# Optimization experiments

Measured on AMD Instinct MI355X. Metric: run time of the kernel, lower is better.

The kernel has to match this reference:

```python
import jax, jax.numpy as jnp
import numpy as np

L, D, H, KV, HD, KVL, I, PL = 8, 2048, 8, 2, 256, 4096, 8192, 256
FULL = (4,)          # layers with full (global) attention / global RoPE
POS = 2047           # current decode position (cache write slot)
N_REP = H // KV      # GQA expansion factor


def rms(x, eps=1e-6):
    # RMSNorm without scale (v_norm); scale applied by caller where needed
    return x * jax.lax.rsqrt(jnp.mean(x * x, axis=-1, keepdims=True) + eps)


def rope(x, cos, sin):
    half = HD // 2
    rot = jnp.concatenate([-x[..., half:], x[..., :half]], axis=-1)
    return x * cos + rot * sin


def _rope_tables(theta):
    inv = 1.0 / (theta ** (np.arange(0, HD, 2, dtype=np.float32) / HD))
    ang = jnp.asarray(POS * inv, dtype=jnp.float32)
    return jnp.concatenate([jnp.cos(ang)] * 2), jnp.concatenate([jnp.sin(ang)] * 2)


def setup_inputs() -> dict:
    key = jax.random.key(0)
    ks = jax.random.split(key, 24)
    r = lambda k, s, sc=0.02: jax.random.normal(k, s, jnp.float32) * sc
    gains = lambda k, s: 1.0 + jax.random.normal(k, s, jnp.float32) * 0.02
    cos_s, sin_s = _rope_tables(10000.0)
    cos_f, sin_f = _rope_tables(1000000.0)
    um = jnp.zeros((1, 1, KVL, 1), jnp.float32).at[0, 0, POS, 0].set(1.0)
    mask = jnp.where(jnp.arange(KVL) <= POS, 0.0, -1e9).astype(jnp.float32)
    return {
        "hidden_states": r(ks[0], (1, 1, D), 1.0),
        "causal_mask": mask,
        "update_mask": um,
        "per_layer_combined": r(ks[1], (1, 1, L * PL), 1.0),
        "cos_s": cos_s, "sin_s": sin_s, "cos_f": cos_f, "sin_f": sin_f,
        "K_in": r(ks[2], (L, KV, KVL, HD)),
        "V_in": r(ks[3], (L, KV, KVL, HD)),
        "w_q": r(ks[4], (L, H * HD, D)),
        "w_k": r(ks[5], (L, KV * HD, D)),
        "w_v": r(ks[6], (L, KV * HD, D)),
        "w_o": r(ks[7], (L, D, H * HD)),
        "g_in_ln": gains(ks[8], (L, D)),
        "g_q_norm": gains(ks[9], (L, HD)),
        "g_k_norm": gains(ks[10], (L, HD)),
        "g_post_attn_ln": gains(ks[11], (L, D)),
        "g_pre_ff_ln": gains(ks[12], (L, D)),
        "g_post_ff_ln": gains(ks[13], (L, D)),
        "w_gate": r(ks[14], (L, I, D)),
        "w_up": r(ks[15], (L, I, D)),
        "w_down": r(ks[16], (L, D, I)),
        "w_plg": r(ks[17], (L, PL, D)),
        "w_plp": r(ks[18], (L, D, PL)),
        "g_post_pl_ln": gains(ks[19], (L, D)),
        "layer_scalar": jnp.ones((L,), jnp.float32),
    }


def reference(hidden_states, causal_mask, update_mask, per_layer_combined,
              cos_s, sin_s, cos_f, sin_f, K_in, V_in,
              w_q, w_k, w_v, w_o,
              g_in_ln, g_q_norm, g_k_norm, g_post_attn_ln, g_pre_ff_ln, g_post_ff_ln,
              w_gate, w_up, w_down, w_plg, w_plp, g_post_pl_ln, layer_scalar):
    um = update_mask[0, 0]          # [KVL,1] one-hot at write position
    h = hidden_states[0, 0]         # [D], batch=1/seq=1 decode
    K_outs, V_outs = [], []
    for i in range(L):
        cos, sin = (cos_f, sin_f) if i in FULL else (cos_s, sin_s)
        # --- attention block ---
        res = h
        x = rms(h) * g_in_ln[i]
        q = rms((w_q[i] @ x).reshape(H, HD)) * g_q_norm[i]
        q = rope(q, cos, sin)                                   # [H,HD]
        k = rms((w_k[i] @ x).reshape(KV, HD)) * g_k_norm[i]
        k = rope(k, cos, sin)                                   # [KV,HD]
        v = rms((w_v[i] @ x).reshape(KV, HD))                    # v_norm (no scale)
        # full-tensor masked blend = KV cache write (faithful to source)
        Ko = K_in[i] * (1.0 - um) + k[:, None, :] * um          # [KV,KVL,HD]
        Vo = V_in[i] * (1.0 - um) + v[:, None, :] * um
        K_outs.append(Ko); V_outs.append(Vo)
        Ke = jnp.repeat(Ko, N_REP, axis=0)                      # GQA expand [H,KVL,HD]
        Ve = jnp.repeat(Vo, N_REP, axis=0)
        scores = jnp.einsum('hd,hkd->hk', q, Ke) + causal_mask  # no 1/sqrt(hd) in source
        attn = jax.nn.softmax(scores, axis=-1)
        ao = jnp.einsum('hk,hkd->hd', attn, Ve).reshape(H * HD)
        ao = rms(w_o[i] @ ao) * g_post_attn_ln[i]
        h = res + ao
        # --- gated MLP ---
        res = h
        xm = rms(h) * g_pre_ff_ln[i]
        m = w_down[i] @ (jax.nn.gelu(w_gate[i] @ xm, approximate=True) * (w_up[i] @ xm))
        h = res + rms(m) * g_post_ff_ln[i]
        # --- per-layer input gating ---
        res = h
        pls = per_layer_combined[0, 0, i * PL:(i + 1) * PL]     # [PL]
        g = jax.nn.gelu(w_plg[i] @ h, approximate=True) * pls
        h = res + rms(w_plp[i] @ g) * g_post_pl_ln[i]
        h = h * layer_scalar[i]
    return (h[None, None, :], jnp.stack(K_outs), jnp.stack(V_outs))
```

## Files before the change

kernel.cpp:

```cpp
#include <hip/hip_runtime.h>

#define NL   8
#define DIM  2048
#define NH   8
#define NKV  2
#define HD   256
#define KVL  4096
#define FFI  8192
#define PLD  256
#define POS  2047
#define NCH  16
#define CP   128

__device__ __forceinline__ float dot4(float4 a, float4 b){
  return a.x*b.x + a.y*b.y + a.z*b.z + a.w*b.w;
}

__device__ __forceinline__ float waveAllSum(float v){
#pragma unroll
  for(int o=1;o<64;o<<=1) v += __shfl_xor(v,o,64);
  return v;
}

__device__ __forceinline__ float waveAllMax(float v){
#pragma unroll
  for(int o=1;o<64;o<<=1) v = fmaxf(v, __shfl_xor(v,o,64));
  return v;
}

__device__ __forceinline__ float blockSum256(float v, float* red){
  int lane = threadIdx.x & 63, w = threadIdx.x >> 6;
  v = waveAllSum(v);
  __syncthreads();
  if(lane==0) red[w] = v;
  __syncthreads();
  return red[0]+red[1]+red[2]+red[3];
}

__device__ __forceinline__ float gelu_tanh(float v){
  return 0.5f*v*(1.0f + tanhf(0.7978845608028654f*(v + 0.044715f*v*v*v)));
}

__global__ __launch_bounds__(256) void qkv_k(
    const float* __restrict__ Wq, const float* __restrict__ Wk,
    const float* __restrict__ Wv,
    const float* __restrict__ hC, const float* __restrict__ u,
    const float* __restrict__ g_pl, const float* __restrict__ lsc,
    const float* __restrict__ g_in, const float* __restrict__ hidden,
    float* __restrict__ hA, float* __restrict__ qkv){
  __shared__ float xs[DIM];
  __shared__ float red[4];
  int tid = threadIdx.x;
  float hv[8];
  if(hidden){
#pragma unroll
    for(int i=0;i<8;i++) hv[i] = hidden[tid + i*256];
  } else {
    float uv[8]; float ss1 = 0.f;
#pragma unroll
    for(int i=0;i<8;i++){ uv[i] = u[tid + i*256]; ss1 += uv[i]*uv[i]; }
    ss1 = blockSum256(ss1, red);
    float r1 = rsqrtf(ss1*(1.f/DIM) + 1e-6f);
    float ls = lsc[0];
#pragma unroll
    for(int i=0;i<8;i++){
      int idx = tid + i*256;
      hv[i] = (hC[idx] + uv[i]*r1*g_pl[idx])*ls;
    }
  }
  float ss2 = 0.f;
#pragma unroll
  for(int i=0;i<8;i++) ss2 += hv[i]*hv[i];
  ss2 = blockSum256(ss2, red);
  float r2 = rsqrtf(ss2*(1.f/DIM) + 1e-6f);
#pragma unroll
  for(int i=0;i<8;i++){
    int idx = tid + i*256;
    xs[idx] = hv[i]*r2*g_in[idx];
    if(blockIdx.x==0) hA[idx] = hv[i];
  }
  __syncthreads();
  int lane = tid & 63, wv = tid >> 6;
  int r = blockIdx.x*4 + wv;
  const float* W; int row;
  if(r < 2048){ W = Wq; row = r; }
  else if(r < 2560){ W = Wk; row = r - 2048; }
  else { W = Wv; row = r - 2560; }
  const float4* Wr = (const float4*)(W + (size_t)row*DIM);
  const float4* xs4 = (const float4*)xs;
  float acc = 0.f;
#pragma unroll
  for(int i=0;i<DIM/256;i++) acc += dot4(Wr[lane + i*64], xs4[lane + i*64]);
  acc = waveAllSum(acc);
  if(lane==0) qkv[r] = acc;
}

__device__ __forceinline__ float4 normRope(const float* __restrict__ raw, int lane,
    const float* __restrict__ gain, const float* __restrict__ cosT,
    const float* __restrict__ sinT, bool doRope){
  float4 v4 = ((const float4*)raw)[lane];
  float ss = waveAllSum(dot4(v4,v4));
  float sc = rsqrtf(ss*(1.f/HD) + 1e-6f);
  float4 n;
  if(gain){
    float4 g4 = ((const float4*)gain)[lane];
    n.x=v4.x*sc*g4.x; n.y=v4.y*sc*g4.y; n.z=v4.z*sc*g4.z; n.w=v4.w*sc*g4.w;
  } else {
    n.x=v4.x*sc; n.y=v4.y*sc; n.z=v4.z*sc; n.w=v4.w*sc;
  }
  if(!doRope) return n;
  float4 np;
  np.x=__shfl_xor(n.x,32,64); np.y=__shfl_xor(n.y,32,64);
  np.z=__shfl_xor(n.z,32,64); np.w=__shfl_xor(n.w,32,64);
  float4 c4 = ((const float4*)cosT)[lane];
  float4 s4 = ((const float4*)sinT)[lane];
  float sg = (lane < 32) ? -1.f : 1.f;
  float4 o;
  o.x = n.x*c4.x + sg*np.x*s4.x;
  o.y = n.y*c4.y + sg*np.y*s4.y;
  o.z = n.z*c4.z + sg*np.z*s4.z;
  o.w = n.w*c4.w + sg*np.w*s4.w;
  return o;
}

__global__ __launch_bounds__(256) void attn_k(
    const float* __restrict__ qkv,
    const float* __restrict__ gq, const float* __restrict__ gk,
    const float* __restrict__ cosT, const float* __restrict__ sinT,
    float* __restrict__ Kc, float* __restrict__ Vc,
    float* __restrict__ pm, float* __restrict__ pl, float* __restrict__ po){
  int b = blockIdx.x;
  int tid = threadIdx.x, lane = tid & 63, wv = tid >> 6;

  if(b == NKV*NCH){
    int kvv = wv >> 1, isV = wv & 1;
    const float* raw = qkv + (isV ? 2560 : 2048) + kvv*HD;
    float4 o = normRope(raw, lane, isV ? nullptr : gk, cosT, sinT, !isV);
    float* dst = (isV ? Vc : Kc) + ((size_t)kvv*KVL + POS)*HD;
    ((float4*)dst)[lane] = o;
    return;
  }

  int kv = b >> 4, c = b & (NCH-1);
  __shared__ float q_s[4][HD];
  __shared__ float kf[HD], vf[HD];
  __shared__ float s_s[4][CP];
  __shared__ float s_w[4][CP];

  {
    float4 o = normRope(qkv + (kv*4 + wv)*HD, lane, gq, cosT, sinT, true);
    ((float4*)q_s[wv])[lane] = o;
  }
  bool fresh = (c == NCH-1);
  if(fresh){
    if(wv == 0){
      float4 o = normRope(qkv + 2048 + kv*HD, lane, gk, cosT, sinT, true);
      ((float4*)kf)[lane] = o;
    } else if(wv == 1){
      float4 o = normRope(qkv + 2560 + kv*HD, lane, nullptr, cosT, sinT, false);
      ((float4*)vf)[lane] = o;
    }
  }
  __syncthreads();

  float4 q4[4];
#pragma unroll
  for(int hh=0;hh<4;hh++) q4[hh] = ((const float4*)q_s[hh])[lane];
  const float4* Kp = (const float4*)(Kc + ((size_t)kv*KVL + c*CP)*HD);
  for(int j=0;j<CP/4;j++){
    int p = wv*(CP/4) + j;
    float4 k4 = (fresh && p==CP-1) ? ((const float4*)kf)[lane]
                                   : Kp[(size_t)p*64 + lane];
    float d0 = dot4(k4,q4[0]), d1 = dot4(k4,q4[1]);
    float d2 = dot4(k4,q4[2]), d3 = dot4(k4,q4[3]);
    d0 = waveAllSum(d0); d1 = waveAllSum(d1);
    d2 = waveAllSum(d2); d3 = waveAllSum(d3);
    if(lane==0){ s_s[0][p]=d0; s_s[1][p]=d1; s_s[2][p]=d2; s_s[3][p]=d3; }
  }
  __syncthreads();

  {
    float s0 = s_s[wv][lane], s1 = s_s[wv][lane+64];
    float m = waveAllMax(fmaxf(s0,s1));
    float e0 = __expf(s0-m), e1 = __expf(s1-m);
    s_w[wv][lane] = e0; s_w[wv][lane+64] = e1;
    float lsum = waveAllSum(e0+e1);
    if(lane==0){
      int hg = kv*4 + wv;
      pm[hg*NCH + c] = m;
      pl[hg*NCH + c] = lsum;
    }
  }
  __syncthreads();

  float acc[4] = {0.f,0.f,0.f,0.f};
  const float* Vp = Vc + ((size_t)kv*KVL + c*CP)*HD;
  for(int p=0;p<CP;p++){
    float vv = (fresh && p==CP-1) ? vf[tid] : Vp[(size_t)p*HD + tid];
#pragma unroll
    for(int hh=0;hh<4;hh++) acc[hh] += s_w[hh][p]*vv;
  }
#pragma unroll
  for(int hh=0;hh<4;hh++){
    int hg = kv*4 + hh;
    po[((size_t)hg*NCH + c)*HD + tid] = acc[hh];
  }
}

__global__ __launch_bounds__(256) void wo_k(const float* __restrict__ W,
    const float* __restrict__ pm, const float* __restrict__ pl,
    const float* __restrict__ po, float* __restrict__ y){
  __shared__ float ao_s[DIM];
  __shared__ float se_s[NH][NCH];
  __shared__ float Ms[NH];
  __shared__ float Li[NH];
  int tid = threadIdx.x;
  if(tid < NH){
    float m = -1e30f;
    for(int c=0;c<NCH;c++) m = fmaxf(m, pm[tid*NCH+c]);
    Ms[tid] = m;
  }
  __syncthreads();
  if(tid < NH*NCH){
    int h = tid >> 4, c = tid & (NCH-1);
    se_s[h][c] = __expf(pm[h*NCH+c] - Ms[h]);
  }
  __syncthreads();
  if(tid < NH){
    float L = 0.f;
    for(int c=0;c<NCH;c++) L += pl[tid*NCH+c]*se_s[tid][c];
    Li[tid] = 1.f/L;
  }
  __syncthreads();
  for(int h=0;h<NH;h++){
    float a = 0.f;
#pragma unroll
    for(int c=0;c<NCH;c++) a += po[((size_t)h*NCH+c)*HD + tid]*se_s[h][c];
    ao_s[h*HD + tid] = a*Li[h];
  }
  __syncthreads();
  int lane = tid & 63, wv = tid >> 6;
  int r = blockIdx.x*4 + wv;
  const float4* Wr = (const float4*)(W + (size_t)r*DIM);
  const float4* xs4 = (const float4*)ao_s;
  float acc = 0.f;
#pragma unroll
  for(int i=0;i<DIM/256;i++) acc += dot4(Wr[lane + i*64], xs4[lane + i*64]);
  acc = waveAllSum(acc);
  if(lane==0) y[r] = acc;
}

__global__ __launch_bounds__(256) void gateup_k(const float* __restrict__ Wg,
    const float* __restrict__ Wu, const float* __restrict__ y,
    const float* __restrict__ hA, const float* __restrict__ g_pa,
    const float* __restrict__ g_pf, float* __restrict__ hB, float* __restrict__ t){
  __shared__ float xs[DIM];
  __shared__ float red[4];
  int tid = threadIdx.x;
  float yv[8]; float ss1 = 0.f;
#pragma unroll
  for(int i=0;i<8;i++){ yv[i] = y[tid + i*256]; ss1 += yv[i]*yv[i]; }
  ss1 = blockSum256(ss1, red);
  float r1 = rsqrtf(ss1*(1.f/DIM) + 1e-6f);
  float hv[8]; float ss2 = 0.f;
#pragma unroll
  for(int i=0;i<8;i++){
    int idx = tid + i*256;
    hv[i] = hA[idx] + yv[i]*r1*g_pa[idx];
    ss2 += hv[i]*hv[i];
  }
  ss2 = blockSum256(ss2, red);
  float r2 = rsqrtf(ss2*(1.f/DIM) + 1e-6f);
#pragma unroll
  for(int i=0;i<8;i++){
    int idx = tid + i*256;
    xs[idx] = hv[i]*r2*g_pf[idx];
    if(blockIdx.x==0) hB[idx] = hv[i];
  }
  __syncthreads();
  int lane = tid & 63, wv = tid >> 6;
  int j = blockIdx.x*4 + wv;
  const float4* Gr = (const float4*)(Wg + (size_t)j*DIM);
  const float4* Ur = (const float4*)(Wu + (size_t)j*DIM);
  const float4* xs4 = (const float4*)xs;
  float ag = 0.f, au = 0.f;
#pragma unroll
  for(int i=0;i<DIM/256;i++){
    float4 bv = xs4[lane + i*64];
    ag += dot4(Gr[lane + i*64], bv);
    au += dot4(Ur[lane + i*64], bv);
  }
  ag = waveAllSum(ag);
  au = waveAllSum(au);
  if(lane==0) t[j] = gelu_tanh(ag)*au;
}

template<int C>
__global__ __launch_bounds__(256) void gemv_k(const float* __restrict__ W,
    const float* __restrict__ x, float* __restrict__ y){
  __shared__ float xs[C];
  for(int i=threadIdx.x; i<C/4; i+=256)
    ((float4*)xs)[i] = ((const float4*)x)[i];
  __syncthreads();
  int lane = threadIdx.x & 63, wv = threadIdx.x >> 6;
  int r = blockIdx.x*4 + wv;
  const float4* Wr = (const float4*)(W + (size_t)r*C);
  const float4* xs4 = (const float4*)xs;
  float acc = 0.f;
#pragma unroll
  for(int i=0;i<C/256;i++) acc += dot4(Wr[lane + i*64], xs4[lane + i*64]);
  acc = waveAllSum(acc);
  if(lane==0) y[r] = acc;
}

__global__ __launch_bounds__(256) void plg_k(const float* __restrict__ W,
    const float* __restrict__ mv, const float* __restrict__ hB,
    const float* __restrict__ g_ff, const float* __restrict__ pls,
    float* __restrict__ hCout, float* __restrict__ gb){
  __shared__ float xs[DIM];
  __shared__ float red[4];
  int tid = threadIdx.x;
  float mvv[8]; float ss1 = 0.f;
#pragma unroll
  for(int i=0;i<8;i++){ mvv[i] = mv[tid + i*256]; ss1 += mvv[i]*mvv[i]; }
  ss1 = blockSum256(ss1, red);
  float r1 = rsqrtf(ss1*(1.f/DIM) + 1e-6f);
#pragma unroll
  for(int i=0;i<8;i++){
    int idx = tid + i*256;
    float hc = hB[idx] + mvv[i]*r1*g_ff[idx];
    xs[idx] = hc;
    if(blockIdx.x==0) hCout[idx] = hc;
  }
  __syncthreads();
  int lane = tid & 63, wv = tid >> 6;
  int r = blockIdx.x*4 + wv;
  const float4* Wr = (const float4*)(W + (size_t)r*DIM);
  const float4* xs4 = (const float4*)xs;
  float acc = 0.f;
#pragma unroll
  for(int i=0;i<DIM/256;i++) acc += dot4(Wr[lane + i*64], xs4[lane + i*64]);
  acc = waveAllSum(acc);
  if(lane==0) gb[r] = gelu_tanh(acc)*pls[r];
}

__global__ __launch_bounds__(256) void final_k(const float* __restrict__ u,
    const float* __restrict__ hC, const float* __restrict__ g_pl,
    const float* __restrict__ lsc, float* __restrict__ out){
  __shared__ float red[4];
  int tid = threadIdx.x;
  float uv[8]; float ss1 = 0.f;
#pragma unroll
  for(int i=0;i<8;i++){ uv[i] = u[tid + i*256]; ss1 += uv[i]*uv[i]; }
  ss1 = blockSum256(ss1, red);
  float r1 = rsqrtf(ss1*(1.f/DIM) + 1e-6f);
  float ls = lsc[0];
#pragma unroll
  for(int i=0;i<8;i++){
    int idx = tid + i*256;
    out[idx] = (hC[idx] + uv[i]*r1*g_pl[idx])*ls;
  }
}

extern "C" void kernel_launch(void* const* d_in, const int* in_sizes, int n_in,
                              void* d_out, int out_size, void* d_ws, size_t ws_size,
                              hipStream_t stream){
  const float* hidden   = (const float*)d_in[0];
  const float* plc      = (const float*)d_in[3];
  const float* cos_s    = (const float*)d_in[4];
  const float* sin_s    = (const float*)d_in[5];
  const float* cos_f    = (const float*)d_in[6];
  const float* sin_f    = (const float*)d_in[7];
  const float* K_in     = (const float*)d_in[8];
  const float* V_in     = (const float*)d_in[9];
  const float* w_q      = (const float*)d_in[10];
  const float* w_k      = (const float*)d_in[11];
  const float* w_v      = (const float*)d_in[12];
  const float* w_o      = (const float*)d_in[13];
  const float* g_in_ln  = (const float*)d_in[14];
  const float* g_q_norm = (const float*)d_in[15];
  const float* g_k_norm = (const float*)d_in[16];
  const float* g_pa_ln  = (const float*)d_in[17];
  const float* g_pf_ln  = (const float*)d_in[18];
  const float* g_ff_ln  = (const float*)d_in[19];
  const float* w_gate   = (const float*)d_in[20];
  const float* w_up     = (const float*)d_in[21];
  const float* w_down   = (const float*)d_in[22];
  const float* w_plg    = (const float*)d_in[23];
  const float* w_plp    = (const float*)d_in[24];
  const float* g_pl_ln  = (const float*)d_in[25];
  const float* l_scal   = (const float*)d_in[26];

  float* out  = (float*)d_out;
  float* outK = out + DIM;
  float* outV = outK + (size_t)NL*NKV*KVL*HD;

  float* ws   = (float*)d_ws;
  float* hA   = ws;
  float* hB   = ws + 2048;
  float* hC   = ws + 4096;
  float* qkv  = ws + 6144;
  float* y    = ws + 9216;
  float* t    = ws + 11264;
  float* mv   = ws + 19456;
  float* gb   = ws + 21504;
  float* u    = ws + 21760;
  float* pm   = ws + 23808;
  float* pl   = ws + 23936;
  float* po   = ws + 24064;

  (void)hipMemcpyAsync(outK, K_in, (size_t)NL*NKV*KVL*HD*sizeof(float),
                       hipMemcpyDeviceToDevice, stream);
  (void)hipMemcpyAsync(outV, V_in, (size_t)NL*NKV*KVL*HD*sizeof(float),
                       hipMemcpyDeviceToDevice, stream);

  for(int l=0;l<NL;l++){
    const float* cosT = (l==4) ? cos_f : cos_s;
    const float* sinT = (l==4) ? sin_f : sin_s;
    float* Kl = outK + (size_t)l*NKV*KVL*HD;
    float* Vl = outV + (size_t)l*NKV*KVL*HD;

    qkv_k<<<768,256,0,stream>>>(
        w_q + (size_t)l*NH*HD*DIM, w_k + (size_t)l*NKV*HD*DIM,
        w_v + (size_t)l*NKV*HD*DIM,
        hC, u,
        (l>0) ? g_pl_ln + (size_t)(l-1)*DIM : g_pl_ln,
        (l>0) ? l_scal + (l-1) : l_scal,
        g_in_ln + (size_t)l*DIM,
        (l==0) ? hidden : nullptr,
        hA, qkv);

    attn_k<<<NKV*NCH+1,256,0,stream>>>(qkv, g_q_norm + l*HD, g_k_norm + l*HD,
                                       cosT, sinT, Kl, Vl, pm, pl, po);

    wo_k<<<512,256,0,stream>>>(w_o + (size_t)l*DIM*NH*HD, pm, pl, po, y);

    gateup_k<<<FFI/4,256,0,stream>>>(w_gate + (size_t)l*FFI*DIM,
                                     w_up + (size_t)l*FFI*DIM,
                                     y, hA, g_pa_ln + (size_t)l*DIM,
                                     g_pf_ln + (size_t)l*DIM, hB, t);

    gemv_k<FFI><<<512,256,0,stream>>>(w_down + (size_t)l*DIM*FFI, t, mv);

    plg_k<<<PLD/4,256,0,stream>>>(w_plg + (size_t)l*PLD*DIM, mv, hB,
                                  g_ff_ln + (size_t)l*DIM, plc + l*PLD, hC, gb);

    gemv_k<PLD><<<512,256,0,stream>>>(w_plp + (size_t)l*DIM*PLD, gb, u);
  }

  final_k<<<1,256,0,stream>>>(u, hC, g_pl_ln + (size_t)(NL-1)*DIM,
                              l_scal + (NL-1), out);
}
```

Measured before the change: 976.5 us.

## Split attention into finer KV chunks, separate combine kernel, prefetch weights in GEMVs

Attention now uses 128 chunks of 16 positions instead of 16 chunks of 128, which gives 257 blocks instead of 33 and spreads KV streaming across more CUs. The cross-chunk softmax combine moves out of wo_k into a new attn_c kernel, and the output projection reuses the generic GEMV. The down projection gets a dedicated kernel with one block per row split across four waves. All GEMVs now load their weight float4s into registers up front to raise memory-level parallelism. The changes add one kernel launch per layer, a larger partial-output buffer and more register pressure.

```diff
diff --git a/kernel.cpp b/kernel.cpp
--- a/kernel.cpp
+++ b/kernel.cpp
@@ -9,8 +9,8 @@
 #define FFI  8192
 #define PLD  256
 #define POS  2047
-#define NCH  16
-#define CP   128
+#define NCH  128
+#define CP   16
 
 __device__ __forceinline__ float dot4(float4 a, float4 b){
   return a.x*b.x + a.y*b.y + a.z*b.z + a.w*b.w;
@@ -19,12 +19,6 @@
 __device__ __forceinline__ float waveAllSum(float v){
 #pragma unroll
   for(int o=1;o<64;o<<=1) v += __shfl_xor(v,o,64);
-  return v;
-}
-
-__device__ __forceinline__ float waveAllMax(float v){
-#pragma unroll
-  for(int o=1;o<64;o<<=1) v = fmaxf(v, __shfl_xor(v,o,64));
   return v;
 }
 
@@ -39,60 +33,6 @@
 
 __device__ __forceinline__ float gelu_tanh(float v){
   return 0.5f*v*(1.0f + tanhf(0.7978845608028654f*(v + 0.044715f*v*v*v)));
-}
-
-__global__ __launch_bounds__(256) void qkv_k(
-    const float* __restrict__ Wq, const float* __restrict__ Wk,
-    const float* __restrict__ Wv,
-    const float* __restrict__ hC, const float* __restrict__ u,
-    const float* __restrict__ g_pl, const float* __restrict__ lsc,
-    const float* __restrict__ g_in, const float* __restrict__ hidden,
-    float* __restrict__ hA, float* __restrict__ qkv){
-  __shared__ float xs[DIM];
-  __shared__ float red[4];
-  int tid = threadIdx.x;
-  float hv[8];
-  if(hidden){
-#pragma unroll
-    for(int i=0;i<8;i++) hv[i] = hidden[tid + i*256];
-  } else {
-    float uv[8]; float ss1 = 0.f;
-#pragma unroll
-    for(int i=0;i<8;i++){ uv[i] = u[tid + i*256]; ss1 += uv[i]*uv[i]; }
-    ss1 = blockSum256(ss1, red);
-    float r1 = rsqrtf(ss1*(1.f/DIM) + 1e-6f);
-    float ls = lsc[0];
-#pragma unroll
-    for(int i=0;i<8;i++){
-      int idx = tid + i*256;
-      hv[i] = (hC[idx] + uv[i]*r1*g_pl[idx])*ls;
-    }
-  }
-  float ss2 = 0.f;
-#pragma unroll
-  for(int i=0;i<8;i++) ss2 += hv[i]*hv[i];
-  ss2 = blockSum256(ss2, red);
-  float r2 = rsqrtf(ss2*(1.f/DIM) + 1e-6f);
-#pragma unroll
-  for(int i=0;i<8;i++){
-    int idx = tid + i*256;
-    xs[idx] = hv[i]*r2*g_in[idx];
-    if(blockIdx.x==0) hA[idx] = hv[i];
-  }
-  __syncthreads();
-  int lane = tid & 63, wv = tid >> 6;
-  int r = blockIdx.x*4 + wv;
-  const float* W; int row;
-  if(r < 2048){ W = Wq; row = r; }
-  else if(r < 2560){ W = Wk; row = r - 2048; }
-  else { W = Wv; row = r - 2560; }
-  const float4* Wr = (const float4*)(W + (size_t)row*DIM);
-  const float4* xs4 = (const float4*)xs;
-  float acc = 0.f;
-#pragma unroll
-  for(int i=0;i<DIM/256;i++) acc += dot4(Wr[lane + i*64], xs4[lane + i*64]);
-  acc = waveAllSum(acc);
-  if(lane==0) qkv[r] = acc;
 }
 
 __device__ __forceinline__ float4 normRope(const float* __restrict__ raw, int lane,
@@ -123,42 +63,97 @@
   return o;
 }
 
+__global__ __launch_bounds__(256) void qkv_k(
+    const float* __restrict__ Wq, const float* __restrict__ Wk,
+    const float* __restrict__ Wv,
+    const float* __restrict__ hC, const float* __restrict__ u,
+    const float* __restrict__ g_pl, const float* __restrict__ lsc,
+    const float* __restrict__ g_in, const float* __restrict__ hidden,
+    float* __restrict__ hA, float* __restrict__ qkv){
+  __shared__ float xs[DIM];
+  __shared__ float red[4];
+  int tid = threadIdx.x;
+  float hv[8];
+  if(hidden){
+#pragma unroll
+    for(int i=0;i<8;i++) hv[i] = hidden[tid + i*256];
+  } else {
+    float uv[8]; float ss1 = 0.f;
+#pragma unroll
+    for(int i=0;i<8;i++){ uv[i] = u[tid + i*256]; ss1 += uv[i]*uv[i]; }
+    ss1 = blockSum256(ss1, red);
+    float r1 = rsqrtf(ss1*(1.f/DIM) + 1e-6f);
+    float ls = lsc[0];
+#pragma unroll
+    for(int i=0;i<8;i++){
+      int idx = tid + i*256;
+      hv[i] = (hC[idx] + uv[i]*r1*g_pl[idx])*ls;
+    }
+  }
+  float ss2 = 0.f;
+#pragma unroll
+  for(int i=0;i<8;i++) ss2 += hv[i]*hv[i];
+  ss2 = blockSum256(ss2, red);
+  float r2 = rsqrtf(ss2*(1.f/DIM) + 1e-6f);
+#pragma unroll
+  for(int i=0;i<8;i++){
+    int idx = tid + i*256;
+    xs[idx] = hv[i]*r2*g_in[idx];
+    if(blockIdx.x==0) hA[idx] = hv[i];
+  }
+  __syncthreads();
+  int lane = tid & 63, wv = tid >> 6;
+  int r = blockIdx.x*4 + wv;
+  const float* W; int row;
+  if(r < 2048){ W = Wq; row = r; }
+  else if(r < 2560){ W = Wk; row = r - 2048; }
+  else { W = Wv; row = r - 2560; }
+  const float4* Wr = (const float4*)(W + (size_t)row*DIM);
+  const float4* xs4 = (const float4*)xs;
+  float4 w8[8];
+#pragma unroll
+  for(int i=0;i<8;i++) w8[i] = Wr[i*64+lane];
+  float acc = 0.f;
+#pragma unroll
+  for(int i=0;i<8;i++) acc += dot4(w8[i], xs4[i*64+lane]);
+  acc = waveAllSum(acc);
+  if(lane==0) qkv[r] = acc;
+}
+
 __global__ __launch_bounds__(256) void attn_k(
-    const float* __restrict__ qkv,
+    const float* __restrict__ qkvb,
     const float* __restrict__ gq, const float* __restrict__ gk,
     const float* __restrict__ cosT, const float* __restrict__ sinT,
-    float* __restrict__ Kc, float* __restrict__ Vc,
+    float* __restrict__ Kl, float* __restrict__ Vl,
     float* __restrict__ pm, float* __restrict__ pl, float* __restrict__ po){
-  int b = blockIdx.x;
-  int tid = threadIdx.x, lane = tid & 63, wv = tid >> 6;
+  int b = blockIdx.x, tid = threadIdx.x, lane = tid & 63, wv = tid >> 6;
 
   if(b == NKV*NCH){
     int kvv = wv >> 1, isV = wv & 1;
-    const float* raw = qkv + (isV ? 2560 : 2048) + kvv*HD;
+    const float* raw = qkvb + (isV ? 2560 : 2048) + kvv*HD;
     float4 o = normRope(raw, lane, isV ? nullptr : gk, cosT, sinT, !isV);
-    float* dst = (isV ? Vc : Kc) + ((size_t)kvv*KVL + POS)*HD;
+    float* dst = (isV ? Vl : Kl) + ((size_t)kvv*KVL + POS)*HD;
     ((float4*)dst)[lane] = o;
     return;
   }
 
-  int kv = b >> 4, c = b & (NCH-1);
+  int kv = b & 1, c = b >> 1;
   __shared__ float q_s[4][HD];
-  __shared__ float kf[HD], vf[HD];
+  __shared__ float vf_s[HD];
   __shared__ float s_s[4][CP];
   __shared__ float s_w[4][CP];
+  bool fresh = (c == NCH-1);
 
   {
-    float4 o = normRope(qkv + (kv*4 + wv)*HD, lane, gq, cosT, sinT, true);
+    float4 o = normRope(qkvb + (kv*4 + wv)*HD, lane, gq, cosT, sinT, true);
     ((float4*)q_s[wv])[lane] = o;
   }
-  bool fresh = (c == NCH-1);
+  float4 kf4 = {0,0,0,0};
   if(fresh){
-    if(wv == 0){
-      float4 o = normRope(qkv + 2048 + kv*HD, lane, gk, cosT, sinT, true);
-      ((float4*)kf)[lane] = o;
-    } else if(wv == 1){
-      float4 o = normRope(qkv + 2560 + kv*HD, lane, nullptr, cosT, sinT, false);
-      ((float4*)vf)[lane] = o;
+    if(wv == 3) kf4 = normRope(qkvb + 2048 + kv*HD, lane, gk, cosT, sinT, true);
+    if(wv == 1){
+      float4 o = normRope(qkvb + 2560 + kv*HD, lane, nullptr, cosT, sinT, false);
+      ((float4*)vf_s)[lane] = o;
     }
   }
   __syncthreads();
@@ -166,11 +161,11 @@
   float4 q4[4];
 #pragma unroll
   for(int hh=0;hh<4;hh++) q4[hh] = ((const float4*)q_s[hh])[lane];
-  const float4* Kp = (const float4*)(Kc + ((size_t)kv*KVL + c*CP)*HD);
-  for(int j=0;j<CP/4;j++){
-    int p = wv*(CP/4) + j;
-    float4 k4 = (fresh && p==CP-1) ? ((const float4*)kf)[lane]
-                                   : Kp[(size_t)p*64 + lane];
+  const float4* Kp = (const float4*)(Kl + ((size_t)kv*KVL + c*CP)*HD);
+#pragma unroll
+  for(int j=0;j<4;j++){
+    int p = wv*4 + j;
+    float4 k4 = (fresh && p==CP-1) ? kf4 : Kp[(size_t)p*64 + lane];
     float d0 = dot4(k4,q4[0]), d1 = dot4(k4,q4[1]);
     float d2 = dot4(k4,q4[2]), d3 = dot4(k4,q4[3]);
     d0 = waveAllSum(d0); d1 = waveAllSum(d1);
@@ -179,73 +174,85 @@
   }
   __syncthreads();
 
-  {
-    float s0 = s_s[wv][lane], s1 = s_s[wv][lane+64];
-    float m = waveAllMax(fmaxf(s0,s1));
-    float e0 = __expf(s0-m), e1 = __expf(s1-m);
-    s_w[wv][lane] = e0; s_w[wv][lane+64] = e1;
-    float lsum = waveAllSum(e0+e1);
-    if(lane==0){
-      int hg = kv*4 + wv;
-      pm[hg*NCH + c] = m;
-      pl[hg*NCH + c] = lsum;
-    }
-  }
-  __syncthreads();
-
+  if(tid < 64){
+    int hh = tid >> 4, pp = tid & 15;
+    float s = s_s[hh][pp];
+    float m = s;
+#pragma unroll
+    for(int o=1;o<16;o<<=1) m = fmaxf(m, __shfl_xor(m,o,64));
+    float e = __expf(s - m);
+    float ls = e;
+#pragma unroll
+    for(int o=1;o<16;o<<=1) ls += __shfl_xor(ls,o,64);
+    s_w[hh][pp] = e;
+    if(pp==0){ int hg = kv*4 + hh; pm[hg*NCH + c] = m; pl[hg*NCH + c] = ls; }
+  }
+  __syncthreads();
+
+  int d = tid;
+  const float* Vp = Vl + ((size_t)kv*KVL + c*CP)*HD;
+  float vv[CP];
+#pragma unroll
+  for(int p2=0;p2<CP;p2++) vv[p2] = Vp[(size_t)p2*HD + d];
+  if(fresh) vv[CP-1] = vf_s[d];
   float acc[4] = {0.f,0.f,0.f,0.f};
-  const float* Vp = Vc + ((size_t)kv*KVL + c*CP)*HD;
-  for(int p=0;p<CP;p++){
-    float vv = (fresh && p==CP-1) ? vf[tid] : Vp[(size_t)p*HD + tid];
-#pragma unroll
-    for(int hh=0;hh<4;hh++) acc[hh] += s_w[hh][p]*vv;
-  }
-#pragma unroll
-  for(int hh=0;hh<4;hh++){
-    int hg = kv*4 + hh;
-    po[((size_t)hg*NCH + c)*HD + tid] = acc[hh];
-  }
-}
-
-__global__ __launch_bounds__(256) void wo_k(const float* __restrict__ W,
-    const float* __restrict__ pm, const float* __restrict__ pl,
-    const float* __restrict__ po, float* __restrict__ y){
-  __shared__ float ao_s[DIM];
-  __shared__ float se_s[NH][NCH];
-  __shared__ float Ms[NH];
-  __shared__ float Li[NH];
-  int tid = threadIdx.x;
-  if(tid < NH){
-    float m = -1e30f;
-    for(int c=0;c<NCH;c++) m = fmaxf(m, pm[tid*NCH+c]);
-    Ms[tid] = m;
-  }
-  __syncthreads();
-  if(tid < NH*NCH){
-    int h = tid >> 4, c = tid & (NCH-1);
-    se_s[h][c] = __expf(pm[h*NCH+c] - Ms[h]);
-  }
-  __syncthreads();
-  if(tid < NH){
-    float L = 0.f;
-    for(int c=0;c<NCH;c++) L += pl[tid*NCH+c]*se_s[tid][c];
-    Li[tid] = 1.f/L;
-  }
-  __syncthreads();
-  for(int h=0;h<NH;h++){
-    float a = 0.f;
-#pragma unroll
-    for(int c=0;c<NCH;c++) a += po[((size_t)h*NCH+c)*HD + tid]*se_s[h][c];
-    ao_s[h*HD + tid] = a*Li[h];
-  }
-  __syncthreads();
-  int lane = tid & 63, wv = tid >> 6;
+#pragma unroll
+  for(int p2=0;p2<CP;p2++){
+#pragma unroll
+    for(int hh=0;hh<4;hh++) acc[hh] += s_w[hh][p2]*vv[p2];
+  }
+#pragma unroll
+  for(int hh=0;hh<4;hh++)
+    po[((size_t)(kv*4+hh)*NCH + c)*HD + d] = acc[hh];
+}
+
+__global__ __launch_bounds__(256) void attn_c(const float* __restrict__ pm,
+    const float* __restrict__ pl, const float* __restrict__ po, float* __restrict__ ao){
+  int h = blockIdx.x, tid = threadIdx.x;
+  __shared__ float sm[NCH], sl[NCH], se[NCH];
+  if(tid < NCH){ sm[tid] = pm[h*NCH+tid]; sl[tid] = pl[h*NCH+tid]; }
+  __syncthreads();
+  float M = -1e30f;
+  for(int c=0;c<NCH;c++) M = fmaxf(M, sm[c]);
+  if(tid < NCH) se[tid] = __expf(sm[tid]-M);
+  __syncthreads();
+  float Lh = 0.f;
+  for(int c=0;c<NCH;c++) Lh += sl[c]*se[c];
+  float a0=0.f, a1=0.f, a2=0.f, a3=0.f;
+#pragma unroll 1
+  for(int c=0;c<NCH;c+=4){
+    a0 += po[((size_t)h*NCH + c  )*HD + tid]*se[c];
+    a1 += po[((size_t)h*NCH + c+1)*HD + tid]*se[c+1];
+    a2 += po[((size_t)h*NCH + c+2)*HD + tid]*se[c+2];
+    a3 += po[((size_t)h*NCH + c+3)*HD + tid]*se[c+3];
+  }
+  ao[h*HD + tid] = (a0+a1+a2+a3) / Lh;
+}
+
+template<int C>
+__global__ __launch_bounds__(256) void gemv_k(const float* __restrict__ W,
+    const float* __restrict__ x, float* __restrict__ y){
+  __shared__ float xs[C];
+  for(int i=threadIdx.x; i<C/4; i+=256)
+    ((float4*)xs)[i] = ((const float4*)x)[i];
+  __syncthreads();
+  int lane = threadIdx.x & 63, wv = threadIdx.x >> 6;
   int r = blockIdx.x*4 + wv;
-  const float4* Wr = (const float4*)(W + (size_t)r*DIM);
-  const float4* xs4 = (const float4*)ao_s;
+  const float4* Wr = (const float4*)(W + (size_t)r*C);
+  const float4* xs4 = (const float4*)xs;
   float acc = 0.f;
 #pragma unroll
-  for(int i=0;i<DIM/256;i++) acc += dot4(Wr[lane + i*64], xs4[lane + i*64]);
+  for(int ii=0;ii<C/2048;ii++){
+    float4 w8[8];
+#pragma unroll
+    for(int i=0;i<8 && ii*8+i < C/256;i++) w8[i] = Wr[(ii*8+i)*64+lane];
+#pragma unroll
+    for(int i=0;i<8 && ii*8+i < C/256;i++) acc += dot4(w8[i], xs4[(ii*8+i)*64+lane]);
+  }
+  if(C < 2048){
+    float4 w1 = Wr[lane];
+    acc = dot4(w1, xs4[lane]);
+  }
   acc = waveAllSum(acc);
   if(lane==0) y[r] = acc;
 }
@@ -283,34 +290,42 @@
   const float4* Gr = (const float4*)(Wg + (size_t)j*DIM);
   const float4* Ur = (const float4*)(Wu + (size_t)j*DIM);
   const float4* xs4 = (const float4*)xs;
+  float4 g8[8], u8[8];
+#pragma unroll
+  for(int i=0;i<8;i++) g8[i] = Gr[i*64+lane];
+#pragma unroll
+  for(int i=0;i<8;i++) u8[i] = Ur[i*64+lane];
   float ag = 0.f, au = 0.f;
 #pragma unroll
-  for(int i=0;i<DIM/256;i++){
-    float4 bv = xs4[lane + i*64];
-    ag += dot4(Gr[lane + i*64], bv);
-    au += dot4(Ur[lane + i*64], bv);
+  for(int i=0;i<8;i++){
+    float4 bv = xs4[i*64+lane];
+    ag += dot4(g8[i], bv);
+    au += dot4(u8[i], bv);
   }
   ag = waveAllSum(ag);
   au = waveAllSum(au);
   if(lane==0) t[j] = gelu_tanh(ag)*au;
 }
 
-template<int C>
-__global__ __launch_bounds__(256) void gemv_k(const float* __restrict__ W,
-    const float* __restrict__ x, float* __restrict__ y){
-  __shared__ float xs[C];
-  for(int i=threadIdx.x; i<C/4; i+=256)
-    ((float4*)xs)[i] = ((const float4*)x)[i];
-  __syncthreads();
-  int lane = threadIdx.x & 63, wv = threadIdx.x >> 6;
-  int r = blockIdx.x*4 + wv;
-  const float4* Wr = (const float4*)(W + (size_t)r*C);
-  const float4* xs4 = (const float4*)xs;
+__global__ __launch_bounds__(256) void down_k(const float* __restrict__ Wd,
+    const float* __restrict__ t, float* __restrict__ mv){
+  __shared__ float red[4];
+  int tid = threadIdx.x, lane = tid & 63, wv = tid >> 6;
+  int r = blockIdx.x;
+  const float4* Wr = (const float4*)(Wd + (size_t)r*FFI) + wv*512;
+  const float4* tp = (const float4*)t + wv*512;
+  float4 w8[8], t8[8];
+#pragma unroll
+  for(int i=0;i<8;i++) w8[i] = Wr[i*64+lane];
+#pragma unroll
+  for(int i=0;i<8;i++) t8[i] = tp[i*64+lane];
   float acc = 0.f;
 #pragma unroll
-  for(int i=0;i<C/256;i++) acc += dot4(Wr[lane + i*64], xs4[lane + i*64]);
+  for(int i=0;i<8;i++) acc += dot4(w8[i], t8[i]);
   acc = waveAllSum(acc);
-  if(lane==0) y[r] = acc;
+  if(lane==0) red[wv] = acc;
+  __syncthreads();
+  if(tid==0) mv[r] = red[0]+red[1]+red[2]+red[3];
 }
 
 __global__ __launch_bounds__(256) void plg_k(const float* __restrict__ W,
@@ -337,9 +352,12 @@
   int r = blockIdx.x*4 + wv;
   const float4* Wr = (const float4*)(W + (size_t)r*DIM);
   const float4* xs4 = (const float4*)xs;
+  float4 w8[8];
+#pragma unroll
+  for(int i=0;i<8;i++) w8[i] = Wr[i*64+lane];
   float acc = 0.f;
 #pragma unroll
-  for(int i=0;i<DIM/256;i++) acc += dot4(Wr[lane + i*64], xs4[lane + i*64]);
+  for(int i=0;i<8;i++) acc += dot4(w8[i], xs4[i*64+lane]);
   acc = waveAllSum(acc);
   if(lane==0) gb[r] = gelu_tanh(acc)*pls[r];
 }
@@ -399,15 +417,16 @@
   float* hA   = ws;
   float* hB   = ws + 2048;
   float* hC   = ws + 4096;
-  float* qkv  = ws + 6144;
+  float* qkvb = ws + 6144;
   float* y    = ws + 9216;
   float* t    = ws + 11264;
   float* mv   = ws + 19456;
   float* gb   = ws + 21504;
   float* u    = ws + 21760;
   float* pm   = ws + 23808;
-  float* pl   = ws + 23936;
-  float* po   = ws + 24064;
+  float* pl   = ws + 24832;
+  float* po   = ws + 25856;
+  float* ao   = ws + 288000;
 
   (void)hipMemcpyAsync(outK, K_in, (size_t)NL*NKV*KVL*HD*sizeof(float),
                        hipMemcpyDeviceToDevice, stream);
@@ -428,19 +447,21 @@
         (l>0) ? l_scal + (l-1) : l_scal,
         g_in_ln + (size_t)l*DIM,
         (l==0) ? hidden : nullptr,
-        hA, qkv);
-
-    attn_k<<<NKV*NCH+1,256,0,stream>>>(qkv, g_q_norm + l*HD, g_k_norm + l*HD,
+        hA, qkvb);
+
+    attn_k<<<NKV*NCH+1,256,0,stream>>>(qkvb, g_q_norm + l*HD, g_k_norm + l*HD,
                                        cosT, sinT, Kl, Vl, pm, pl, po);
 
-    wo_k<<<512,256,0,stream>>>(w_o + (size_t)l*DIM*NH*HD, pm, pl, po, y);
+    attn_c<<<NH,256,0,stream>>>(pm, pl, po, ao);
+
+    gemv_k<DIM><<<512,256,0,stream>>>(w_o + (size_t)l*DIM*NH*HD, ao, y);
 
     gateup_k<<<FFI/4,256,0,stream>>>(w_gate + (size_t)l*FFI*DIM,
                                      w_up + (size_t)l*FFI*DIM,
                                      y, hA, g_pa_ln + (size_t)l*DIM,
                                      g_pf_ln + (size_t)l*DIM, hB, t);
 
-    gemv_k<FFI><<<512,256,0,stream>>>(w_down + (size_t)l*DIM*FFI, t, mv);
+    down_k<<<DIM,256,0,stream>>>(w_down + (size_t)l*DIM*FFI, t, mv);
 
     plg_k<<<PLD/4,256,0,stream>>>(w_plg + (size_t)l*PLD*DIM, mv, hB,
                                   g_ff_ln + (size_t)l*DIM, plc + l*PLD, hC, gb);
```

Result: faster. 809.2 us (-17.1%).
